# Kernel tuning notes

Measured on AMD Instinct MI355X. Metric: run time of the kernel, lower is better.

## Reference

```python
import jax, jax.numpy as jnp
import numpy as np

B, L_IMG, L_TXT = 2, 1024, 512
D_IMG, D_TXT = 2048, 1024
NH, NKV, HD = 16, 8, 128
MLP_IMG, MLP_TXT = 8192, 4096
SOFTCAP = 50.0
EPS = 1e-6

def rms_norm(x, scale):
    var = jnp.mean(jnp.square(x), axis=-1, keepdims=True)
    return x * jax.lax.rsqrt(var + EPS) * (1.0 + scale)

def rope(x, positions):
    # x: [B, L, N, H]; positions: [B, L]
    H = x.shape[-1]
    half = H // 2
    freq = jnp.exp(-jnp.log(10000.0) * (jnp.arange(half, dtype=jnp.float32) * 2.0 / H))
    theta = positions[:, :, None].astype(jnp.float32) * freq          # [B, L, half]
    sin = jnp.sin(theta)[:, :, None, :]
    cos = jnp.cos(theta)[:, :, None, :]
    x1, x2 = jnp.split(x, 2, axis=-1)
    return jnp.concatenate([x1 * cos - x2 * sin, x2 * cos + x1 * sin], axis=-1).astype(x.dtype)

def get_qkv(x_norm, positions, wq, wk, wv):
    b, l, _ = x_norm.shape
    q = (x_norm @ wq).reshape(b, l, NH, HD)
    k = (x_norm @ wk).reshape(b, l, NKV, HD)
    v = (x_norm @ wv).reshape(b, l, NKV, HD)
    q = rope(q, positions)
    k = rope(k, positions)
    q = q * (HD ** -0.5)  # query_pre_attn_norm = 'rsqrt_head_dim'
    return q, k, v

def joint_attention(q, k, v, mask):
    # q: [B,T,NH,HD]; k,v: [B,S,NKV,HD]; mask: [B,1,T,S] bool
    b, t, n, h = q.shape
    g = n // NKV
    qg = q.reshape(b, t, NKV, g, h)
    logits = jnp.einsum('btkgh,bskh->bkgts', qg, k)
    logits = jnp.tanh(logits / SOFTCAP) * SOFTCAP  # attn_logits_softcap
    logits = jnp.where(mask[:, :, None], logits, -1e30)  # [B,1,1,T,S] broadcast
    probs = jax.nn.softmax(logits, axis=-1)
    out = jnp.einsum('bkgts,bskh->btkgh', probs, v)
    return out.reshape(b, t, n, h)

def ffn(x, w_gate, w_up, w_down):
    return (jax.nn.gelu(x @ w_gate) * (x @ w_up)) @ w_down

def _mixture_post(attn_proj, residual, pre_ffw_scale, w_gate, w_up, w_down):
    # post_norms=False, dropout=0: h = mlp(norm(attn_proj + x)) + x
    h = attn_proj + residual
    h = rms_norm(h, pre_ffw_scale)
    h = ffn(h, w_gate, w_up, w_down)
    return h + residual

def _block(x_img, x_txt, attn_mask,
           img_pre_attn_scale, img_wq, img_wk, img_wv, img_wo,
           img_pre_ffw_scale, img_w_gate, img_w_up, img_w_down,
           txt_pre_attn_scale, txt_wq, txt_wk, txt_wv, txt_wo,
           txt_pre_ffw_scale, txt_w_gate, txt_w_up, txt_w_down):
    pos_img = jnp.arange(0, L_IMG, dtype=jnp.int32)[None, :]
    pos_txt = jnp.arange(L_IMG, L_IMG + L_TXT, dtype=jnp.int32)[None, :]
    qi, ki, vi = get_qkv(rms_norm(x_img, img_pre_attn_scale), pos_img, img_wq, img_wk, img_wv)
    qt, kt, vt = get_qkv(rms_norm(x_txt, txt_pre_attn_scale), pos_txt, txt_wq, txt_wk, txt_wv)
    q = jnp.concatenate([qi, qt], axis=1)
    k = jnp.concatenate([ki, kt], axis=1)
    v = jnp.concatenate([vi, vt], axis=1)
    attn = joint_attention(q, k, v, attn_mask)  # [B, T, NH, HD]
    b = attn.shape[0]
    attn_flat = attn.reshape(b, L_IMG + L_TXT, NH * HD)
    proj_img = attn_flat[:, :L_IMG, :] @ img_wo
    proj_txt = attn_flat[:, L_IMG:, :] @ txt_wo
    out_img = _mixture_post(proj_img, x_img, img_pre_ffw_scale, img_w_gate, img_w_up, img_w_down)
    out_txt = _mixture_post(proj_txt, x_txt, txt_pre_ffw_scale, txt_w_gate, txt_w_up, txt_w_down)
    return out_img, out_txt

def setup_inputs() -> dict:
    key = jax.random.key(0)
    ks = jax.random.split(key, 32)
    inner = NH * HD
    def w(k, shape, fan_in):
        return jax.random.normal(k, shape, dtype=jnp.float32) / np.sqrt(fan_in)
    inp = {
        'x_img': jax.random.normal(ks[0], (B, L_IMG, D_IMG), dtype=jnp.float32),
        'x_txt': jax.random.normal(ks[1], (B, L_TXT, D_TXT), dtype=jnp.float32),
        'attn_mask': jnp.ones((B, 1, L_IMG + L_TXT, L_IMG + L_TXT), dtype=bool),
        'img_pre_attn_scale': jnp.zeros((D_IMG,), jnp.float32),
        'img_wq': w(ks[2], (D_IMG, inner), D_IMG),
        'img_wk': w(ks[3], (D_IMG, NKV * HD), D_IMG),
        'img_wv': w(ks[4], (D_IMG, NKV * HD), D_IMG),
        'img_wo': w(ks[5], (inner, D_IMG), inner),
        'img_pre_ffw_scale': jnp.zeros((D_IMG,), jnp.float32),
        'img_w_gate': w(ks[6], (D_IMG, MLP_IMG), D_IMG),
        'img_w_up': w(ks[7], (D_IMG, MLP_IMG), D_IMG),
        'img_w_down': w(ks[8], (MLP_IMG, D_IMG), MLP_IMG),
        'txt_pre_attn_scale': jnp.zeros((D_TXT,), jnp.float32),
        'txt_wq': w(ks[9], (D_TXT, inner), D_TXT),
        'txt_wk': w(ks[10], (D_TXT, NKV * HD), D_TXT),
        'txt_wv': w(ks[11], (D_TXT, NKV * HD), D_TXT),
        'txt_wo': w(ks[12], (inner, D_TXT), inner),
        'txt_pre_ffw_scale': jnp.zeros((D_TXT,), jnp.float32),
        'txt_w_gate': w(ks[13], (D_TXT, MLP_TXT), D_TXT),
        'txt_w_up': w(ks[14], (D_TXT, MLP_TXT), D_TXT),
        'txt_w_down': w(ks[15], (MLP_TXT, D_TXT), MLP_TXT),
    }
    return inp

def reference(x_img, x_txt, attn_mask,
              img_pre_attn_scale, img_wq, img_wk, img_wv, img_wo,
              img_pre_ffw_scale, img_w_gate, img_w_up, img_w_down,
              txt_pre_attn_scale, txt_wq, txt_wk, txt_wv, txt_wo,
              txt_pre_ffw_scale, txt_w_gate, txt_w_up, txt_w_down):
    return _block(x_img, x_txt, attn_mask,
                  img_pre_attn_scale, img_wq, img_wk, img_wv, img_wo,
                  img_pre_ffw_scale, img_w_gate, img_w_up, img_w_down,
                  txt_pre_attn_scale, txt_wq, txt_wk, txt_wv, txt_wo,
                  txt_pre_ffw_scale, txt_w_gate, txt_w_up, txt_w_down)
```

## Files before the change

### kernel.cpp

```cpp
#include <hip/hip_runtime.h>
#include <hip/hip_bf16.h>


typedef __hip_bfloat16 bf16;
typedef __attribute__((ext_vector_type(8))) __bf16 bf16x8;
typedef __attribute__((ext_vector_type(4))) float f32x4;

#define DEV __device__ __forceinline__

static constexpr int TT = 1536;
static constexpr int NHQ = 16, NKVH = 8, HDM = 128;

DEV void async_load16(const void* g, void* l) {
  typedef const __attribute__((address_space(1))) void* gas_t;
  typedef __attribute__((address_space(3))) void* las_t;
  __builtin_amdgcn_global_load_lds((gas_t)g, (las_t)l, 16, 0, 0);
}

DEV f32x4 mfma16(bf16x8 a, bf16x8 b, f32x4 c) {
  return __builtin_amdgcn_mfma_f32_16x16x32_bf16(a, b, c, 0, 0, 0);
}

DEV float bf2f(bf16 x) { return __bfloat162float(x); }
DEV bf16  f2bf(float x) { return __float2bfloat16(x); }

struct TJob { const float* src; bf16* dst; int K; int N; };
struct TJobs { TJob j[14]; int cum[15]; };

__global__ __launch_bounds__(256) void wt_transpose(TJobs P) {
  __shared__ bf16 tile[64][65];
  int bid = blockIdx.x;
  int ji = 0;
  while (ji < 13 && bid >= P.cum[ji + 1]) ji++;
  const TJob jb = P.j[ji];
  int rel = bid - P.cum[ji];
  int ntc = jb.N >> 6;
  int tr = rel / ntc, tc = rel - tr * ntc;
  int r0 = tr << 6, c0 = tc << 6;
  int t = threadIdx.x;
  #pragma unroll
  for (int i = 0; i < 16; i++) {
    int idx = i * 256 + t;
    int r = idx >> 6, c = idx & 63;
    tile[c][r] = f2bf(jb.src[(size_t)(r0 + r) * jb.N + c0 + c]);
  }
  __syncthreads();
  #pragma unroll
  for (int i = 0; i < 16; i++) {
    int idx = i * 256 + t;
    int r = idx >> 6, c = idx & 63;
    jb.dst[(size_t)(c0 + r) * jb.K + r0 + c] = tile[r][c];
  }
}

__global__ __launch_bounds__(256) void transpose_v(const bf16* __restrict__ v_all,
                                                   bf16* __restrict__ vt) {
  int st = blockIdx.x, ht = blockIdx.y, bk = blockIdx.z;
  int b = bk >> 3, kv = bk & 7;
  __shared__ bf16 tile[64][65];
  int t = threadIdx.x;
  int s0 = st * 64, h0 = ht * 64;
  #pragma unroll
  for (int i = 0; i < 16; i++) {
    int idx = i * 256 + t;
    int r = idx >> 6, c = idx & 63;
    tile[c][r] = v_all[((size_t)(b * TT + s0 + r) * NKVH + kv) * HDM + h0 + c];
  }
  __syncthreads();
  #pragma unroll
  for (int i = 0; i < 16; i++) {
    int idx = i * 256 + t;
    int r = idx >> 6, c = idx & 63;
    vt[((size_t)bk * HDM + h0 + r) * TT + s0 + c] = tile[r][c];
  }
}

template <int DV>
__global__ __launch_bounds__(256) void rmsnorm_k(const float* __restrict__ x,
                                                 const float* __restrict__ sc,
                                                 bf16* __restrict__ out) {
  const int D = DV * 1024;
  int row = blockIdx.x, t = threadIdx.x;
  const float4* xr = reinterpret_cast<const float4*>(x + (size_t)row * D);
  float4 v[DV];
  float ss = 0.f;
  #pragma unroll
  for (int i = 0; i < DV; i++) {
    v[i] = xr[t + i * 256];
    ss += v[i].x * v[i].x + v[i].y * v[i].y + v[i].z * v[i].z + v[i].w * v[i].w;
  }
  #pragma unroll
  for (int o = 1; o < 64; o <<= 1) ss += __shfl_xor(ss, o);
  __shared__ float red[4];
  if ((t & 63) == 0) red[t >> 6] = ss;
  __syncthreads();
  float r = rsqrtf((red[0] + red[1] + red[2] + red[3]) * (1.0f / D) + 1e-6f);
  bf16* orow = out + (size_t)row * D;
  #pragma unroll
  for (int i = 0; i < DV; i++) {
    int c = (t + i * 256) * 4;
    orow[c + 0] = f2bf(v[i].x * r * (1.f + sc[c + 0]));
    orow[c + 1] = f2bf(v[i].y * r * (1.f + sc[c + 1]));
    orow[c + 2] = f2bf(v[i].z * r * (1.f + sc[c + 2]));
    orow[c + 3] = f2bf(v[i].w * r * (1.f + sc[c + 3]));
  }
}

__global__ __launch_bounds__(256) void rope_inplace(bf16* __restrict__ x, int lognh,
                                                    float scale) {
  int gid = blockIdx.x * 256 + threadIdx.x;
  int i = gid & 63;
  int rh = gid >> 6;
  int row = rh >> lognh;
  int pos = row >= TT ? row - TT : row;
  float fr = expf(-9.210340371976184f * ((float)(2 * i) * (1.0f / 128.0f)));
  float th = (float)pos * fr;
  float s, c;
  sincosf(th, &s, &c);
  bf16* p = x + (size_t)rh * HDM;
  float x1 = bf2f(p[i]), x2 = bf2f(p[i + 64]);
  p[i]      = f2bf((x1 * c - x2 * s) * scale);
  p[i + 64] = f2bf((x2 * c + x1 * s) * scale);
}

struct G8Job {
  const bf16* A; const bf16* B; bf16* Cb; float* Cf;
  int K, N, lda, ldb;
  int a_base, a_lsh, a_lskip;
  int c_base, c_lsh, c_lskip, c_stride;
};
struct G8Jobs { G8Job j[6]; int cum[7]; int nj; };

#define G8_BAR_MFMA(MH, NH)                                        \
  __builtin_amdgcn_s_barrier();                                    \
  asm volatile("s_waitcnt lgkmcnt(0)" ::: "memory");               \
  __builtin_amdgcn_sched_barrier(0);                               \
  __builtin_amdgcn_s_setprio(1);                                   \
  _Pragma("unroll")                                                \
  for (int i = 0; i < 4; i++)                                      \
    _Pragma("unroll")                                              \
    for (int nj2 = 0; nj2 < 2; nj2++)                              \
      _Pragma("unroll")                                            \
      for (int kk = 0; kk < 2; kk++)                               \
        acc[(MH)*4 + i][(NH)*2 + nj2] = mfma16(                    \
            afr[i][kk], bfr[(NH)*2 + nj2][kk],                     \
            acc[(MH)*4 + i][(NH)*2 + nj2]);                        \
  __builtin_amdgcn_s_setprio(0);                                   \
  __builtin_amdgcn_s_barrier();                                    \
  asm volatile("" ::: "memory");

__global__ __launch_bounds__(512, 2) void gemm8(G8Jobs P) {
  extern __shared__ __align__(16) bf16 lds8[];
  int bid = blockIdx.x;
  int ji = 0;
  while (ji < P.nj - 1 && bid >= P.cum[ji + 1]) ji++;
  const G8Job jb = P.j[ji];
  int rel = bid - P.cum[ji];
  int tn = jb.N >> 8;
  int bm = rel / tn, bn = rel - bm * tn;
  const int m0 = bm << 8, n0 = bn << 8;
  const int K = jb.K;
  const int nk = K >> 6;

  const int tid = threadIdx.x;
  const int w = tid >> 6, l = tid & 63;
  const int lr = l & 15, lk = l >> 4;
  const int wr = w >> 2, wc = w & 3;

  const int r0 = tid >> 3, sl0 = (tid & 7) ^ (r0 & 7);
  const int dst0 = (w * 64) * 8;
  const int dst1 = (512 + w * 64) * 8;

  auto stage = [&](int ht, int hq) {
    int k0 = ht << 6;
    bf16* ldsb = lds8 + ((ht & 1) * 32768 + hq * 8192);
    if (hq < 2) {
      int ma = m0 + hq * 128;
      int mr0 = ma + r0, mr1 = ma + 64 + r0;
      int pr0 = jb.a_base + mr0 + ((mr0 >> jb.a_lsh) * jb.a_lskip);
      int pr1 = jb.a_base + mr1 + ((mr1 >> jb.a_lsh) * jb.a_lskip);
      async_load16(jb.A + (size_t)pr0 * jb.lda + k0 + sl0 * 8, ldsb + dst0);
      async_load16(jb.A + (size_t)pr1 * jb.lda + k0 + sl0 * 8, ldsb + dst1);
    } else {
      int nb = n0 + (hq - 2) * 128;
      async_load16(jb.B + (size_t)(nb + r0) * jb.ldb + k0 + sl0 * 8, ldsb + dst0);
      async_load16(jb.B + (size_t)(nb + 64 + r0) * jb.ldb + k0 + sl0 * 8, ldsb + dst1);
    }
  };

  f32x4 acc[8][4];
  #pragma unroll
  for (int i = 0; i < 8; i++)
    #pragma unroll
    for (int j = 0; j < 4; j++) acc[i][j] = (f32x4){0.f, 0.f, 0.f, 0.f};

  const int s0 = ((0 * 4 + lk) ^ (lr & 7)) * 8;
  const int s1 = ((1 * 4 + lk) ^ (lr & 7)) * 8;
  const int browb = (wc & 1) * 64;

  #pragma unroll
  for (int hq = 0; hq < 4; hq++) stage(0, hq);
  #pragma unroll
  for (int hq = 0; hq < 4; hq++) stage(1, hq);
  asm volatile("s_waitcnt vmcnt(8)" ::: "memory");
  __builtin_amdgcn_s_barrier();
  asm volatile("" ::: "memory");

  bf16x8 afr[4][2], bfr[4][2];

  for (int t = 0; t < nk; t++) {
    const bf16* bufA = lds8 + (t & 1) * 32768 + wr * 8192;
    const bf16* bufB = lds8 + (t & 1) * 32768 + 16384 + (wc >> 1) * 8192;
    const bool st = (t + 2 < nk);

    #pragma unroll
    for (int i = 0; i < 4; i++) {
      int rb = (i * 16 + lr) * 64;
      afr[i][0] = *reinterpret_cast<const bf16x8*>(bufA + rb + s0);
      afr[i][1] = *reinterpret_cast<const bf16x8*>(bufA + rb + s1);
    }
    #pragma unroll
    for (int ni = 0; ni < 2; ni++) {
      int rb = (browb + ni * 16 + lr) * 64;
      bfr[ni][0] = *reinterpret_cast<const bf16x8*>(bufB + rb + s0);
      bfr[ni][1] = *reinterpret_cast<const bf16x8*>(bufB + rb + s1);
    }
    G8_BAR_MFMA(0, 0)

    #pragma unroll
    for (int ni = 2; ni < 4; ni++) {
      int rb = (browb + ni * 16 + lr) * 64;
      bfr[ni][0] = *reinterpret_cast<const bf16x8*>(bufB + rb + s0);
      bfr[ni][1] = *reinterpret_cast<const bf16x8*>(bufB + rb + s1);
    }
    G8_BAR_MFMA(0, 1)

    #pragma unroll
    for (int i = 0; i < 4; i++) {
      int rb = ((i + 4) * 16 + lr) * 64;
      afr[i][0] = *reinterpret_cast<const bf16x8*>(bufA + rb + s0);
      afr[i][1] = *reinterpret_cast<const bf16x8*>(bufA + rb + s1);
    }
    if (st) { stage(t + 2, 2); stage(t + 2, 3); }
    G8_BAR_MFMA(1, 0)

    if (st) {
      stage(t + 2, 0); stage(t + 2, 1);
      asm volatile("s_waitcnt vmcnt(8)" ::: "memory");
    } else if (t == nk - 2) {
      asm volatile("s_waitcnt vmcnt(0)" ::: "memory");
    }
    G8_BAR_MFMA(1, 1)
  }

  if (jb.Cf) {
    #pragma unroll
    for (int mi = 0; mi < 8; mi++)
      #pragma unroll
      for (int jj = 0; jj < 4; jj++) {
        int m = m0 + wr * 128 + mi * 16 + lk * 4 + jj;
        float* drow = jb.Cf + (size_t)m * jb.c_stride + n0 + wc * 64;
        #pragma unroll
        for (int ni = 0; ni < 4; ni++) drow[ni * 16 + lr] = acc[mi][ni][jj];
      }
  } else {
    #pragma unroll
    for (int mi = 0; mi < 8; mi++)
      #pragma unroll
      for (int jj = 0; jj < 4; jj++) {
        int m = m0 + wr * 128 + mi * 16 + lk * 4 + jj;
        int crow = jb.c_base + m + ((m >> jb.c_lsh) * jb.c_lskip);
        bf16* drow = jb.Cb + (size_t)crow * jb.c_stride + n0 + wc * 64;
        #pragma unroll
        for (int ni = 0; ni < 4; ni++) drow[ni * 16 + lr] = f2bf(acc[mi][ni][jj]);
      }
  }
}

__global__ __launch_bounds__(256) void reduce_add(
    float* __restrict__ d0, const float* __restrict__ p0, const float* __restrict__ r0,
    int n40,
    float* __restrict__ d1, const float* __restrict__ p1, const float* __restrict__ r1,
    int n41) {
  int tot = n40 + n41;
  for (int idx = blockIdx.x * 256 + threadIdx.x; idx < tot; idx += gridDim.x * 256) {
    if (idx < n40) {
      float4 d = ((const float4*)d0)[idx];
      float4 p = ((const float4*)p0)[idx];
      float4 r = ((const float4*)r0)[idx];
      ((float4*)d0)[idx] = make_float4(d.x + p.x + r.x, d.y + p.y + r.y,
                                       d.z + p.z + r.z, d.w + p.w + r.w);
    } else {
      int i = idx - n40;
      float4 d = ((const float4*)d1)[i];
      float4 p = ((const float4*)p1)[i];
      float4 r = ((const float4*)r1)[i];
      ((float4*)d1)[i] = make_float4(d.x + p.x + r.x, d.y + p.y + r.y,
                                     d.z + p.z + r.z, d.w + p.w + r.w);
    }
  }
}

__global__ __launch_bounds__(256) void gelu_mul(bf16* __restrict__ gu_i,
                                                bf16* __restrict__ gu_t) {
  const int IMG_CH = 2048 * 8192 / 8;
  const int TXT_CH = 1024 * 4096 / 8;
  int idx = blockIdx.x * 256 + threadIdx.x;
  int total = IMG_CH + TXT_CH;
  if (idx >= total) return;
  bf16* base;
  int half, ci;
  if (idx < IMG_CH) { base = gu_i; half = 8192; ci = idx; }
  else              { base = gu_t; half = 4096; ci = idx - IMG_CH; }
  int rowlen = half * 2;
  int perrow = half / 8;
  int m = ci / perrow, n8 = ci - m * perrow;
  bf16* gp = base + (size_t)m * rowlen + n8 * 8;
  bf16* up = gp + half;
  bf16x8 g8 = *reinterpret_cast<const bf16x8*>(gp);
  bf16x8 u8 = *reinterpret_cast<const bf16x8*>(up);
  bf16x8 o8;
  #pragma unroll
  for (int i = 0; i < 8; i++) {
    float g = (float)g8[i], u = (float)u8[i];
    float t = tanhf(0.7978845608028654f * (g + 0.044715f * g * g * g));
    o8[i] = (__bf16)(0.5f * g * (1.f + t) * u);
  }
  *reinterpret_cast<bf16x8*>(gp) = o8;
}

__global__ __launch_bounds__(256) void attn_k(const bf16* __restrict__ q_all,
                                              const bf16* __restrict__ k_all,
                                              const bf16* __restrict__ vt,
                                              bf16* __restrict__ attn_o) {
  const int qt = blockIdx.x;
  const int n = blockIdx.y;
  const int b = blockIdx.z;
  const int kv = n >> 1;
  const int tid = threadIdx.x, w = tid >> 6, l = tid & 63;
  const int lr = l & 15, lk = l >> 4;
  __shared__ __align__(16) bf16 Ksm[64 * 128];
  __shared__ __align__(16) bf16 Vsm[128 * 64];
  __shared__ __align__(16) bf16 Psm[4][16][72];

  bf16x8 qf[4];
  {
    int t = qt * 64 + w * 16 + lr;
    const bf16* qp = q_all + ((size_t)(b * TT + t) * NHQ + n) * HDM;
    #pragma unroll
    for (int kk = 0; kk < 4; kk++)
      qf[kk] = *reinterpret_cast<const bf16x8*>(qp + kk * 32 + lk * 8);
  }
  f32x4 acc_o[8];
  #pragma unroll
  for (int i = 0; i < 8; i++) acc_o[i] = (f32x4){0.f, 0.f, 0.f, 0.f};
  float den[4] = {0.f, 0.f, 0.f, 0.f};

  for (int st = 0; st < TT / 64; st++) {
    __syncthreads();
    #pragma unroll
    for (int i = 0; i < 4; i++) {
      int cb = (w * 4 + i) * 64;
      int c = cb + l;
      {
        int srow = c >> 4, c16 = c & 15;
        const bf16* g = k_all + ((size_t)(b * TT + st * 64 + srow) * NKVH + kv) * HDM +
                        ((c16 ^ (srow & 7)) << 3);
        async_load16(g, Ksm + cb * 8);
      }
      {
        int hrow = c >> 3, c8 = c & 7;
        const bf16* g = vt + ((size_t)(b * NKVH + kv) * HDM + hrow) * TT + st * 64 +
                        ((c8 ^ (hrow & 7)) << 3);
        async_load16(g, Vsm + cb * 8);
      }
    }
    __syncthreads();
    #pragma unroll
    for (int sf = 0; sf < 4; sf++) {
      f32x4 s4 = (f32x4){0.f, 0.f, 0.f, 0.f};
      int sl = sf * 16 + lr;
      #pragma unroll
      for (int kk = 0; kk < 4; kk++) {
        int e = kk * 32 + lk * 8;
        bf16x8 kf = *reinterpret_cast<const bf16x8*>(
            Ksm + sl * 128 + ((((e >> 3) ^ (sl & 7))) << 3));
        s4 = mfma16(qf[kk], kf, s4);
      }
      #pragma unroll
      for (int j = 0; j < 4; j++) {
        float xv = s4[j];
        float tcap = tanhf(xv * 0.02f) * 50.f;
        float p = __expf(tcap);
        Psm[w][lk * 4 + j][sf * 16 + lr] = f2bf(p);
        p += __shfl_xor(p, 1);
        p += __shfl_xor(p, 2);
        p += __shfl_xor(p, 4);
        p += __shfl_xor(p, 8);
        den[j] += p;
      }
    }
    #pragma unroll
    for (int kk2 = 0; kk2 < 2; kk2++) {
      bf16x8 pa = *reinterpret_cast<const bf16x8*>(&Psm[w][lr][kk2 * 32 + lk * 8]);
      #pragma unroll
      for (int hf = 0; hf < 8; hf++) {
        int h = hf * 16 + lr;
        int e2 = kk2 * 32 + lk * 8;
        bf16x8 vb = *reinterpret_cast<const bf16x8*>(
            Vsm + h * 64 + ((((e2 >> 3) ^ (h & 7))) << 3));
        acc_o[hf] = mfma16(pa, vb, acc_o[hf]);
      }
    }
  }
  #pragma unroll
  for (int hf = 0; hf < 8; hf++)
    #pragma unroll
    for (int j = 0; j < 4; j++) {
      int t = qt * 64 + w * 16 + lk * 4 + j;
      float val = acc_o[hf][j] / den[j];
      attn_o[((size_t)(b * TT + t)) * (NHQ * HDM) + n * HDM + hf * 16 + lr] = f2bf(val);
    }
}

extern "C" void kernel_launch(void* const* d_in, const int* in_sizes, int n_in,
                              void* d_out, int out_size, void* d_ws,
                              size_t ws_size, hipStream_t stream) {
  const float* x_img = (const float*)d_in[0];
  const float* x_txt = (const float*)d_in[1];
  const float* sc_attn_i = (const float*)d_in[3];
  const float* wq_i = (const float*)d_in[4];
  const float* wk_i = (const float*)d_in[5];
  const float* wv_i = (const float*)d_in[6];
  const float* wo_i = (const float*)d_in[7];
  const float* sc_ffw_i = (const float*)d_in[8];
  const float* wg_i = (const float*)d_in[9];
  const float* wu_i = (const float*)d_in[10];
  const float* wd_i = (const float*)d_in[11];
  const float* sc_attn_t = (const float*)d_in[12];
  const float* wq_t = (const float*)d_in[13];
  const float* wk_t = (const float*)d_in[14];
  const float* wv_t = (const float*)d_in[15];
  const float* wo_t = (const float*)d_in[16];
  const float* sc_ffw_t = (const float*)d_in[17];
  const float* wg_t = (const float*)d_in[18];
  const float* wu_t = (const float*)d_in[19];
  const float* wd_t = (const float*)d_in[20];
  float* outp = (float*)d_out;
  float* outp_t = outp + (size_t)2 * 1024 * 2048;

  char* ws = (char*)d_ws;
  size_t off = 0;
  auto alloc = [&](size_t n) {
    char* p = ws + off;
    off += (n + 255) & ~(size_t)255;
    return p;
  };
  bf16* WqT_i = (bf16*)alloc((size_t)2048 * 2048 * 2);
  bf16* WkT_i = (bf16*)alloc((size_t)1024 * 2048 * 2);
  bf16* WvT_i = (bf16*)alloc((size_t)1024 * 2048 * 2);
  bf16* WoT_i = (bf16*)alloc((size_t)2048 * 2048 * 2);
  bf16* WguT_i = (bf16*)alloc((size_t)16384 * 2048 * 2);
  bf16* WdT_i = (bf16*)alloc((size_t)2048 * 8192 * 2);
  bf16* WqT_t = (bf16*)alloc((size_t)2048 * 1024 * 2);
  bf16* WkT_t = (bf16*)alloc((size_t)1024 * 1024 * 2);
  bf16* WvT_t = (bf16*)alloc((size_t)1024 * 1024 * 2);
  bf16* WoT_t = (bf16*)alloc((size_t)1024 * 2048 * 2);
  bf16* WguT_t = (bf16*)alloc((size_t)8192 * 1024 * 2);
  bf16* WdT_t = (bf16*)alloc((size_t)1024 * 4096 * 2);
  bf16* xn_i = (bf16*)alloc((size_t)2048 * 2048 * 2);
  bf16* xn_t = (bf16*)alloc((size_t)1024 * 1024 * 2);
  float* h_i = (float*)alloc((size_t)2048 * 2048 * 4);
  float* h_t = (float*)alloc((size_t)1024 * 1024 * 4);
  char* S = (char*)alloc((size_t)84 * 1024 * 1024);
  (void)ws_size;
  bf16* q_all = (bf16*)S;
  bf16* k_all = (bf16*)(S + 12582912);
  bf16* v_all = (bf16*)(S + 18874368);
  bf16* vtr   = (bf16*)(S + 25165824);
  bf16* attn_o= (bf16*)(S + 31457280);
  float* p1wo_i = (float*)S;
  float* p1wo_t = (float*)(S + 16777216);
  bf16* gu_i  = (bf16*)S;
  bf16* gu_t  = (bf16*)(S + (size_t)2048 * 16384 * 2);
  float* p1dn_i = (float*)xn_i;
  float* p1dn_t = (float*)((char*)xn_i + 16777216);

  (void)hipFuncSetAttribute(reinterpret_cast<const void*>(gemm8),
                            hipFuncAttributeMaxDynamicSharedMemorySize, 131072);

  TJobs tj;
  auto setj = [&](int idx, const float* s, bf16* d, int K, int N) {
    tj.j[idx].src = s; tj.j[idx].dst = d; tj.j[idx].K = K; tj.j[idx].N = N;
  };
  setj(0, wq_i, WqT_i, 2048, 2048);
  setj(1, wk_i, WkT_i, 2048, 1024);
  setj(2, wv_i, WvT_i, 2048, 1024);
  setj(3, wo_i, WoT_i, 2048, 2048);
  setj(4, wg_i, WguT_i, 2048, 8192);
  setj(5, wu_i, WguT_i + (size_t)8192 * 2048, 2048, 8192);
  setj(6, wd_i, WdT_i, 8192, 2048);
  setj(7, wq_t, WqT_t, 1024, 2048);
  setj(8, wk_t, WkT_t, 1024, 1024);
  setj(9, wv_t, WvT_t, 1024, 1024);
  setj(10, wo_t, WoT_t, 2048, 1024);
  setj(11, wg_t, WguT_t, 1024, 4096);
  setj(12, wu_t, WguT_t + (size_t)4096 * 1024, 1024, 4096);
  setj(13, wd_t, WdT_t, 4096, 1024);
  tj.cum[0] = 0;
  for (int i = 0; i < 14; i++)
    tj.cum[i + 1] = tj.cum[i] + (tj.j[i].K >> 6) * (tj.j[i].N >> 6);
  wt_transpose<<<tj.cum[14], 256, 0, stream>>>(tj);

  rmsnorm_k<2><<<2048, 256, 0, stream>>>(x_img, sc_attn_i, xn_i);
  rmsnorm_k<1><<<1024, 256, 0, stream>>>(x_txt, sc_attn_t, xn_t);

  auto mk8b = [](const bf16* A, const bf16* B, bf16* Cb, int K, int N, int lda,
                 int ldb, int ab, int ash, int ask, int cb2, int csh, int csk,
                 int cstr) {
    G8Job g{};
    g.A = A; g.B = B; g.Cb = Cb; g.Cf = nullptr;
    g.K = K; g.N = N; g.lda = lda; g.ldb = ldb;
    g.a_base = ab; g.a_lsh = ash; g.a_lskip = ask;
    g.c_base = cb2; g.c_lsh = csh; g.c_lskip = csk; g.c_stride = cstr;
    return g;
  };
  auto mk8f = [](const bf16* A, const bf16* B, float* Cf, int K, int N, int lda,
                 int ldb, int ab, int ash, int ask, int cstr) {
    G8Job g{};
    g.A = A; g.B = B; g.Cb = nullptr; g.Cf = Cf;
    g.K = K; g.N = N; g.lda = lda; g.ldb = ldb;
    g.a_base = ab; g.a_lsh = ash; g.a_lskip = ask;
    g.c_base = 0; g.c_lsh = 30; g.c_lskip = 0; g.c_stride = cstr;
    return g;
  };
  auto launch8 = [&](G8Jobs& P, int nj, const int* Mt) {
    P.nj = nj;
    P.cum[0] = 0;
    for (int i = 0; i < nj; i++) P.cum[i + 1] = P.cum[i] + Mt[i] * (P.j[i].N >> 8);
    gemm8<<<P.cum[nj], 512, 131072, stream>>>(P);
  };

  {
    G8Jobs P;
    P.j[0] = mk8b(xn_i, WqT_i, q_all, 2048, 2048, 2048, 2048, 0, 30, 0, 0, 10, 512, 2048);
    P.j[1] = mk8b(xn_i, WkT_i, k_all, 2048, 1024, 2048, 2048, 0, 30, 0, 0, 10, 512, 1024);
    P.j[2] = mk8b(xn_i, WvT_i, v_all, 2048, 1024, 2048, 2048, 0, 30, 0, 0, 10, 512, 1024);
    P.j[3] = mk8b(xn_t, WqT_t, q_all, 1024, 2048, 1024, 1024, 0, 30, 0, 1024, 9, 1024, 2048);
    P.j[4] = mk8b(xn_t, WkT_t, k_all, 1024, 1024, 1024, 1024, 0, 30, 0, 1024, 9, 1024, 1024);
    P.j[5] = mk8b(xn_t, WvT_t, v_all, 1024, 1024, 1024, 1024, 0, 30, 0, 1024, 9, 1024, 1024);
    int Mt[6] = {8, 8, 8, 4, 4, 4};
    launch8(P, 6, Mt);
  }

  rope_inplace<<<12288, 256, 0, stream>>>(q_all, 4, 0.08838834764831845f);
  rope_inplace<<<6144, 256, 0, stream>>>(k_all, 3, 1.0f);

  transpose_v<<<dim3(24, 2, 16), 256, 0, stream>>>(v_all, vtr);

  attn_k<<<dim3(24, 16, 2), 256, 0, stream>>>(q_all, k_all, vtr, attn_o);

  {
    G8Jobs P;
    P.j[0] = mk8f(attn_o,        WoT_i,        h_i,    1024, 2048, 2048, 2048, 0, 10, 512, 2048);
    P.j[1] = mk8f(attn_o + 1024, WoT_i + 1024, p1wo_i, 1024, 2048, 2048, 2048, 0, 10, 512, 2048);
    P.j[2] = mk8f(attn_o,        WoT_t,        h_t,    1024, 1024, 2048, 2048, 1024, 9, 1024, 1024);
    P.j[3] = mk8f(attn_o + 1024, WoT_t + 1024, p1wo_t, 1024, 1024, 2048, 2048, 1024, 9, 1024, 1024);
    int Mt[4] = {8, 8, 4, 4};
    launch8(P, 4, Mt);
    reduce_add<<<2048, 256, 0, stream>>>(h_i, p1wo_i, x_img, 2048 * 2048 / 4,
                                         h_t, p1wo_t, x_txt, 1024 * 1024 / 4);
  }

  rmsnorm_k<2><<<2048, 256, 0, stream>>>(h_i, sc_ffw_i, xn_i);
  rmsnorm_k<1><<<1024, 256, 0, stream>>>(h_t, sc_ffw_t, xn_t);

  {
    G8Jobs P;
    P.j[0] = mk8b(xn_i, WguT_i, gu_i, 2048, 16384, 2048, 2048, 0, 30, 0, 0, 30, 0, 16384);
    P.j[1] = mk8b(xn_t, WguT_t, gu_t, 1024, 8192, 1024, 1024, 0, 30, 0, 0, 30, 0, 8192);
    int Mt[2] = {8, 4};
    launch8(P, 2, Mt);
  }
  {
    int total = 2048 * 8192 / 8 + 1024 * 4096 / 8;
    gelu_mul<<<(total + 255) / 256, 256, 0, stream>>>(gu_i, gu_t);
  }

  {
    G8Jobs P;
    P.j[0] = mk8f(gu_i,        WdT_i,        outp,   4096, 2048, 16384, 8192, 0, 30, 0, 2048);
    P.j[1] = mk8f(gu_i + 4096, WdT_i + 4096, p1dn_i, 4096, 2048, 16384, 8192, 0, 30, 0, 2048);
    P.j[2] = mk8f(gu_t,        WdT_t,        outp_t, 2048, 1024, 8192,  4096, 0, 30, 0, 1024);
    P.j[3] = mk8f(gu_t + 2048, WdT_t + 2048, p1dn_t, 2048, 1024, 8192,  4096, 0, 30, 0, 1024);
    int Mt[4] = {8, 8, 4, 4};
    launch8(P, 4, Mt);
    reduce_add<<<2048, 256, 0, stream>>>(outp, p1dn_i, x_img, 2048 * 2048 / 4,
                                         outp_t, p1dn_t, x_txt, 1024 * 1024 / 4);
  }
}
```

Before: 665.6 us.

## Increase split-K for Wo and down GEMMs, fuse residual reduce into RMSNorm

Result: slower. 688.4 us (+3.4%).

```diff
diff --git a/kernel.cpp b/kernel.cpp
--- a/kernel.cpp
+++ b/kernel.cpp
@@ -87,6 +87,47 @@
   #pragma unroll
   for (int i = 0; i < DV; i++) {
     v[i] = xr[t + i * 256];
+    ss += v[i].x * v[i].x + v[i].y * v[i].y + v[i].z * v[i].z + v[i].w * v[i].w;
+  }
+  #pragma unroll
+  for (int o = 1; o < 64; o <<= 1) ss += __shfl_xor(ss, o);
+  __shared__ float red[4];
+  if ((t & 63) == 0) red[t >> 6] = ss;
+  __syncthreads();
+  float r = rsqrtf((red[0] + red[1] + red[2] + red[3]) * (1.0f / D) + 1e-6f);
+  bf16* orow = out + (size_t)row * D;
+  #pragma unroll
+  for (int i = 0; i < DV; i++) {
+    int c = (t + i * 256) * 4;
+    orow[c + 0] = f2bf(v[i].x * r * (1.f + sc[c + 0]));
+    orow[c + 1] = f2bf(v[i].y * r * (1.f + sc[c + 1]));
+    orow[c + 2] = f2bf(v[i].z * r * (1.f + sc[c + 2]));
+    orow[c + 3] = f2bf(v[i].w * r * (1.f + sc[c + 3]));
+  }
+}
+
+template <int DV>
+__global__ __launch_bounds__(256) void rmsnorm4_k(
+    const float* __restrict__ p0, const float* __restrict__ p1,
+    const float* __restrict__ p2, const float* __restrict__ p3,
+    const float* __restrict__ x, const float* __restrict__ sc,
+    bf16* __restrict__ out) {
+  const int D = DV * 1024;
+  int row = blockIdx.x, t = threadIdx.x;
+  size_t rb = (size_t)row * (D / 4);
+  const float4* r0 = reinterpret_cast<const float4*>(p0) + rb;
+  const float4* r1 = reinterpret_cast<const float4*>(p1) + rb;
+  const float4* r2 = reinterpret_cast<const float4*>(p2) + rb;
+  const float4* r3 = reinterpret_cast<const float4*>(p3) + rb;
+  const float4* xr = reinterpret_cast<const float4*>(x) + rb;
+  float4 v[DV];
+  float ss = 0.f;
+  #pragma unroll
+  for (int i = 0; i < DV; i++) {
+    int idx = t + i * 256;
+    float4 a = r0[idx], b = r1[idx], c = r2[idx], d = r3[idx], e = xr[idx];
+    v[i] = make_float4(a.x + b.x + c.x + d.x + e.x, a.y + b.y + c.y + d.y + e.y,
+                       a.z + b.z + c.z + d.z + e.z, a.w + b.w + c.w + d.w + e.w);
     ss += v[i].x * v[i].x + v[i].y * v[i].y + v[i].z * v[i].z + v[i].w * v[i].w;
   }
   #pragma unroll
@@ -129,7 +170,7 @@
   int a_base, a_lsh, a_lskip;
   int c_base, c_lsh, c_lskip, c_stride;
 };
-struct G8Jobs { G8Job j[6]; int cum[7]; int nj; };
+struct G8Jobs { G8Job j[8]; int cum[9]; int nj; };
 
 #define G8_BAR_MFMA(MH, NH)                                        \
   __builtin_amdgcn_s_barrier();                                    \
@@ -277,46 +318,53 @@
   }
 }
 
-__global__ __launch_bounds__(256) void reduce_add(
-    float* __restrict__ d0, const float* __restrict__ p0, const float* __restrict__ r0,
-    int n40,
-    float* __restrict__ d1, const float* __restrict__ p1, const float* __restrict__ r1,
-    int n41) {
-  int tot = n40 + n41;
+__global__ __launch_bounds__(256) void reduce_down(
+    float* __restrict__ oi, const float* __restrict__ q1,
+    const float* __restrict__ q2, const float* __restrict__ q3,
+    const float* __restrict__ xi, int n4i,
+    float* __restrict__ ot, const float* __restrict__ r1,
+    const float* __restrict__ xt, int n4t) {
+  int tot = n4i + n4t;
   for (int idx = blockIdx.x * 256 + threadIdx.x; idx < tot; idx += gridDim.x * 256) {
-    if (idx < n40) {
-      float4 d = ((const float4*)d0)[idx];
-      float4 p = ((const float4*)p0)[idx];
-      float4 r = ((const float4*)r0)[idx];
-      ((float4*)d0)[idx] = make_float4(d.x + p.x + r.x, d.y + p.y + r.y,
-                                       d.z + p.z + r.z, d.w + p.w + r.w);
+    if (idx < n4i) {
+      float4 d = ((const float4*)oi)[idx];
+      float4 a = ((const float4*)q1)[idx];
+      float4 b = ((const float4*)q2)[idx];
+      float4 c = ((const float4*)q3)[idx];
+      float4 e = ((const float4*)xi)[idx];
+      ((float4*)oi)[idx] = make_float4(d.x + a.x + b.x + c.x + e.x,
+                                       d.y + a.y + b.y + c.y + e.y,
+                                       d.z + a.z + b.z + c.z + e.z,
+                                       d.w + a.w + b.w + c.w + e.w);
     } else {
-      int i = idx - n40;
-      float4 d = ((const float4*)d1)[i];
-      float4 p = ((const float4*)p1)[i];
-      float4 r = ((const float4*)r1)[i];
-      ((float4*)d1)[i] = make_float4(d.x + p.x + r.x, d.y + p.y + r.y,
-                                     d.z + p.z + r.z, d.w + p.w + r.w);
-    }
-  }
-}
-
-__global__ __launch_bounds__(256) void gelu_mul(bf16* __restrict__ gu_i,
-                                                bf16* __restrict__ gu_t) {
+      int i = idx - n4i;
+      float4 d = ((const float4*)ot)[i];
+      float4 a = ((const float4*)r1)[i];
+      float4 e = ((const float4*)xt)[i];
+      ((float4*)ot)[i] = make_float4(d.x + a.x + e.x, d.y + a.y + e.y,
+                                     d.z + a.z + e.z, d.w + a.w + e.w);
+    }
+  }
+}
+
+__global__ __launch_bounds__(256) void gelu_mul(const bf16* __restrict__ gu_i,
+                                                bf16* __restrict__ act_i,
+                                                const bf16* __restrict__ gu_t,
+                                                bf16* __restrict__ act_t) {
   const int IMG_CH = 2048 * 8192 / 8;
   const int TXT_CH = 1024 * 4096 / 8;
   int idx = blockIdx.x * 256 + threadIdx.x;
   int total = IMG_CH + TXT_CH;
   if (idx >= total) return;
-  bf16* base;
+  const bf16* base;
+  bf16* abase;
   int half, ci;
-  if (idx < IMG_CH) { base = gu_i; half = 8192; ci = idx; }
-  else              { base = gu_t; half = 4096; ci = idx - IMG_CH; }
-  int rowlen = half * 2;
+  if (idx < IMG_CH) { base = gu_i; abase = act_i; half = 8192; ci = idx; }
+  else              { base = gu_t; abase = act_t; half = 4096; ci = idx - IMG_CH; }
   int perrow = half / 8;
   int m = ci / perrow, n8 = ci - m * perrow;
-  bf16* gp = base + (size_t)m * rowlen + n8 * 8;
-  bf16* up = gp + half;
+  const bf16* gp = base + (size_t)m * (half * 2) + n8 * 8;
+  const bf16* up = gp + half;
   bf16x8 g8 = *reinterpret_cast<const bf16x8*>(gp);
   bf16x8 u8 = *reinterpret_cast<const bf16x8*>(up);
   bf16x8 o8;
@@ -326,7 +374,7 @@
     float t = tanhf(0.7978845608028654f * (g + 0.044715f * g * g * g));
     o8[i] = (__bf16)(0.5f * g * (1.f + t) * u);
   }
-  *reinterpret_cast<bf16x8*>(gp) = o8;
+  *reinterpret_cast<bf16x8*>(abase + (size_t)m * half + n8 * 8) = o8;
 }
 
 __global__ __launch_bounds__(256) void attn_k(const bf16* __restrict__ q_all,
@@ -470,21 +518,28 @@
   bf16* WdT_t = (bf16*)alloc((size_t)1024 * 4096 * 2);
   bf16* xn_i = (bf16*)alloc((size_t)2048 * 2048 * 2);
   bf16* xn_t = (bf16*)alloc((size_t)1024 * 1024 * 2);
-  float* h_i = (float*)alloc((size_t)2048 * 2048 * 4);
-  float* h_t = (float*)alloc((size_t)1024 * 1024 * 4);
-  char* S = (char*)alloc((size_t)84 * 1024 * 1024);
+  char* S = (char*)alloc((size_t)112 * 1024 * 1024);
   (void)ws_size;
+
+  const size_t MB = 1024 * 1024;
   bf16* q_all = (bf16*)S;
-  bf16* k_all = (bf16*)(S + 12582912);
-  bf16* v_all = (bf16*)(S + 18874368);
-  bf16* vtr   = (bf16*)(S + 25165824);
-  bf16* attn_o= (bf16*)(S + 31457280);
-  float* p1wo_i = (float*)S;
-  float* p1wo_t = (float*)(S + 16777216);
+  bf16* k_all = (bf16*)(S + 12 * MB);
+  bf16* v_all = (bf16*)(S + 18 * MB);
+  bf16* vtr   = (bf16*)(S + 24 * MB);
+  bf16* attn_o= (bf16*)(S + 30 * MB);
+  float* wp0 = (float*)(S + 42 * MB);
+  float* wp1 = (float*)(S + 62 * MB);
+  float* wp2 = (float*)(S + 82 * MB);
+  float* wp3 = (float*)S;
+  const size_t TXT_OFF = 16 * MB / 4;
   bf16* gu_i  = (bf16*)S;
-  bf16* gu_t  = (bf16*)(S + (size_t)2048 * 16384 * 2);
-  float* p1dn_i = (float*)xn_i;
-  float* p1dn_t = (float*)((char*)xn_i + 16777216);
+  bf16* gu_t  = (bf16*)(S + 64 * MB);
+  bf16* act_i = (bf16*)(S + 80 * MB);
+  bf16* act_t = (bf16*)xn_i;
+  float* dp1 = (float*)S;
+  float* dp2 = (float*)(S + 16 * MB);
+  float* dp3 = (float*)(S + 32 * MB);
+  float* dpt = (float*)(S + 48 * MB);
 
   (void)hipFuncSetAttribute(reinterpret_cast<const void*>(gemm8),
                             hipFuncAttributeMaxDynamicSharedMemorySize, 131072);
@@ -562,40 +617,50 @@
 
   {
     G8Jobs P;
-    P.j[0] = mk8f(attn_o,        WoT_i,        h_i,    1024, 2048, 2048, 2048, 0, 10, 512, 2048);
-    P.j[1] = mk8f(attn_o + 1024, WoT_i + 1024, p1wo_i, 1024, 2048, 2048, 2048, 0, 10, 512, 2048);
-    P.j[2] = mk8f(attn_o,        WoT_t,        h_t,    1024, 1024, 2048, 2048, 1024, 9, 1024, 1024);
-    P.j[3] = mk8f(attn_o + 1024, WoT_t + 1024, p1wo_t, 1024, 1024, 2048, 2048, 1024, 9, 1024, 1024);
-    int Mt[4] = {8, 8, 4, 4};
-    launch8(P, 4, Mt);
-    reduce_add<<<2048, 256, 0, stream>>>(h_i, p1wo_i, x_img, 2048 * 2048 / 4,
-                                         h_t, p1wo_t, x_txt, 1024 * 1024 / 4);
-  }
-
-  rmsnorm_k<2><<<2048, 256, 0, stream>>>(h_i, sc_ffw_i, xn_i);
-  rmsnorm_k<1><<<1024, 256, 0, stream>>>(h_t, sc_ffw_t, xn_t);
+    float* wp[4] = {wp0, wp1, wp2, wp3};
+    for (int s = 0; s < 4; s++) {
+      P.j[s] = mk8f(attn_o + s * 512, WoT_i + s * 512, wp[s], 512, 2048, 2048,
+                    2048, 0, 10, 512, 2048);
+      P.j[4 + s] = mk8f(attn_o + s * 512, WoT_t + s * 512, wp[s] + TXT_OFF, 512,
+                        1024, 2048, 2048, 1024, 9, 1024, 1024);
+    }
+    int Mt[8] = {8, 8, 8, 8, 4, 4, 4, 4};
+    launch8(P, 8, Mt);
+  }
+
+  rmsnorm4_k<2><<<2048, 256, 0, stream>>>(wp0, wp1, wp2, wp3, x_img, sc_ffw_i, xn_i);
+  rmsnorm4_k<1><<<1024, 256, 0, stream>>>(wp0 + TXT_OFF, wp1 + TXT_OFF,
+                                          wp2 + TXT_OFF, wp3 + TXT_OFF, x_txt,
+                                          sc_ffw_t, xn_t);
 
   {
     G8Jobs P;
     P.j[0] = mk8b(xn_i, WguT_i, gu_i, 2048, 16384, 2048, 2048, 0, 30, 0, 0, 30, 0, 16384);
-    P.j[1] = mk8b(xn_t, WguT_t, gu_t, 1024, 8192, 1024, 1024, 0, 30, 0, 0, 30, 0, 8192);
-    int Mt[2] = {8, 4};
-    launch8(P, 2, Mt);
+    int Mt[1] = {8};
+    launch8(P, 1, Mt);
+  }
+  {
+    G8Jobs P;
+    P.j[0] = mk8b(xn_t, WguT_t, gu_t, 1024, 8192, 1024, 1024, 0, 30, 0, 0, 30, 0, 8192);
+    int Mt[1] = {4};
+    launch8(P, 1, Mt);
   }
   {
     int total = 2048 * 8192 / 8 + 1024 * 4096 / 8;
-    gelu_mul<<<(total + 255) / 256, 256, 0, stream>>>(gu_i, gu_t);
+    gelu_mul<<<(total + 255) / 256, 256, 0, stream>>>(gu_i, act_i, gu_t, act_t);
   }
 
   {
     G8Jobs P;
-    P.j[0] = mk8f(gu_i,        WdT_i,        outp,   4096, 2048, 16384, 8192, 0, 30, 0, 2048);
-    P.j[1] = mk8f(gu_i + 4096, WdT_i + 4096, p1dn_i, 4096, 2048, 16384, 8192, 0, 30, 0, 2048);
-    P.j[2] = mk8f(gu_t,        WdT_t,        outp_t, 2048, 1024, 8192,  4096, 0, 30, 0, 1024);
-    P.j[3] = mk8f(gu_t + 2048, WdT_t + 2048, p1dn_t, 2048, 1024, 8192,  4096, 0, 30, 0, 1024);
-    int Mt[4] = {8, 8, 4, 4};
-    launch8(P, 4, Mt);
-    reduce_add<<<2048, 256, 0, stream>>>(outp, p1dn_i, x_img, 2048 * 2048 / 4,
-                                         outp_t, p1dn_t, x_txt, 1024 * 1024 / 4);
-  }
-}
+    P.j[0] = mk8f(act_i,            WdT_i,            outp, 2048, 2048, 8192, 8192, 0, 30, 0, 2048);
+    P.j[1] = mk8f(act_i + 2048,     WdT_i + 2048,     dp1,  2048, 2048, 8192, 8192, 0, 30, 0, 2048);
+    P.j[2] = mk8f(act_i + 4096,     WdT_i + 4096,     dp2,  2048, 2048, 8192, 8192, 0, 30, 0, 2048);
+    P.j[3] = mk8f(act_i + 6144,     WdT_i + 6144,     dp3,  2048, 2048, 8192, 8192, 0, 30, 0, 2048);
+    P.j[4] = mk8f(act_t,            WdT_t,            outp_t, 2048, 1024, 4096, 4096, 0, 30, 0, 1024);
+    P.j[5] = mk8f(act_t + 2048,     WdT_t + 2048,     dpt,  2048, 1024, 4096, 4096, 0, 30, 0, 1024);
+    int Mt[6] = {8, 8, 8, 8, 4, 4};
+    launch8(P, 6, Mt);
+  }
+  reduce_down<<<2048, 256, 0, stream>>>(outp, dp1, dp2, dp3, x_img, 2048 * 2048 / 4,
+                                        outp_t, dpt, x_txt, 1024 * 1024 / 4);
+}
```
